# Optimization experiments

Hardware: AMD Instinct MI355X
Metric: run time of the kernel (lower is better)

## Reference

```python
import jax, jax.numpy as jnp
import numpy as np

X_DIM = 1024
HEADS = 16
EPS = 1e-5  # torch LayerNorm default


def setup_inputs() -> dict:
    key = jax.random.key(0)
    ks = jax.random.split(key, 4)
    B, N = 4, 1024
    x = jax.random.normal(ks[0], (B, N, X_DIM), jnp.float32)
    # torch nn.Linear weights are [out_features, in_features]; y = x @ W.T
    Wq = jax.random.normal(ks[1], (X_DIM, X_DIM), jnp.float32) * 0.02
    Wkv = jax.random.normal(ks[2], (2 * X_DIM, X_DIM), jnp.float32) * 0.02  # k_dim = x_dim + v_dim
    Wt = jax.random.normal(ks[3], (HEADS, HEADS), jnp.float32) * 0.25  # talk_h head-mixing
    ln_g = jnp.ones((HEADS,), jnp.float32)
    ln_b = jnp.zeros((HEADS,), jnp.float32)
    return {"x": x, "Wq": Wq, "Wkv": Wkv, "Wt": Wt, "ln_g": ln_g, "ln_b": ln_b}


def reference(x, Wq, Wkv, Wt, ln_g, ln_b):
    B, N, D = x.shape
    H = HEADS
    dh = D // H  # v head dim (= x head dim here since v_dim == x_dim)
    # projections
    q = (x @ Wq.T).reshape(B, N, H, dh).transpose(0, 2, 1, 3)  # b h i d
    kv = x @ Wkv.T  # [B, N, 2D]
    k = kv[..., :D].reshape(B, N, H, dh).transpose(0, 2, 1, 3)  # b h j d
    v = kv[..., D:].reshape(B, N, H, dh).transpose(0, 2, 1, 3)  # b h j d
    # scaled dot-product scores (scale uses x_dim, not head dim — faithful to source)
    dots = jnp.einsum('bhid,bhjd->bhij', q, k) * (D ** -0.5)
    w = jax.nn.softmax(dots, axis=-1)  # [B, H, N, N]
    # talk_h: ChSwap (transpose dims 1 and -1) -> Linear(heads) -> LayerNorm(heads) -> ChSwap
    wt = w.transpose(0, 3, 2, 1)  # b j i h
    wt = wt @ Wt.T
    mu = wt.mean(-1, keepdims=True)
    var = wt.var(-1, keepdims=True)
    wt = (wt - mu) / jnp.sqrt(var + EPS) * ln_g + ln_b
    w = wt.transpose(0, 3, 2, 1)  # back to b h i j
    # soft attention output
    attn = jnp.einsum('bhij,bhjd->bhid', w, v)
    # hard selection: argmax over keys, gather value rows
    idx = jnp.argmax(w, axis=-1)  # [B, H, N]
    hard = jnp.take_along_axis(v, jnp.broadcast_to(idx[..., None], idx.shape + (dh,)), axis=2)
    # straight-through: forward = hard, gradient flows through attn
    rtn = attn - jax.lax.stop_gradient(attn - hard)
    return rtn.transpose(0, 2, 1, 3).reshape(B, N, H * dh)
```

## Files before the change

kernel.cpp:

```cpp
#include <hip/hip_runtime.h>


#define FMA4(cc, av, bv) \
  cc.x = fmaf(av, bv.x, cc.x); cc.y = fmaf(av, bv.y, cc.y); \
  cc.z = fmaf(av, bv.z, cc.z); cc.w = fmaf(av, bv.w, cc.w);

__global__ __launch_bounds__(256) void qkv_gemm(
    const float* __restrict__ X, const float* __restrict__ Wq,
    const float* __restrict__ Wkv, float* __restrict__ qT,
    float* __restrict__ kT, float* __restrict__ V)
{
  __shared__ __align__(16) float As[16 * 132];
  __shared__ __align__(16) float Bs[16 * 132];
  __shared__ __align__(16) float tb[128 * 32];

  const int t  = threadIdx.x;
  const int bn = blockIdx.x;
  const int bm = blockIdx.y;
  const int m0 = bm * 128, n0 = bn * 128;
  const int ty = t >> 4, tx = t & 15;

  const float* Wbase = (n0 < 1024) ? Wq : Wkv;
  const int nw0 = (n0 < 1024) ? n0 : (n0 - 1024);

  float4 c2[8][2];
#pragma unroll
  for (int a = 0; a < 8; a++) {
    c2[a][0] = make_float4(0.f, 0.f, 0.f, 0.f);
    c2[a][1] = make_float4(0.f, 0.f, 0.f, 0.f);
  }

  const int lr = t >> 1;
  const int lh = t & 1;

  const float4* As4 = (const float4*)As;
  const float4* Bs4 = (const float4*)Bs;

  for (int kb = 0; kb < 64; kb++) {
    const int k0 = kb * 16;
    __syncthreads();
#pragma unroll
    for (int s = 0; s < 2; s++) {
      const int kk = lh * 8 + s * 4;
      float4 av = *(const float4*)&X[(size_t)(m0 + lr) * 1024 + k0 + kk];
      float4 bv = *(const float4*)&Wbase[(size_t)(nw0 + lr) * 1024 + k0 + kk];
      As[(kk + 0) * 132 + lr] = av.x;
      As[(kk + 1) * 132 + lr] = av.y;
      As[(kk + 2) * 132 + lr] = av.z;
      As[(kk + 3) * 132 + lr] = av.w;
      Bs[(kk + 0) * 132 + lr] = bv.x;
      Bs[(kk + 1) * 132 + lr] = bv.y;
      Bs[(kk + 2) * 132 + lr] = bv.z;
      Bs[(kk + 3) * 132 + lr] = bv.w;
    }
    __syncthreads();
#pragma unroll
    for (int kk = 0; kk < 16; kk++) {
      float4 a0 = As4[kk * 33 + ty * 2];
      float4 a1 = As4[kk * 33 + ty * 2 + 1];
      float4 b0 = Bs4[kk * 33 + tx];
      float4 b1 = Bs4[kk * 33 + 16 + tx];
      FMA4(c2[0][0], a0.x, b0); FMA4(c2[0][1], a0.x, b1);
      FMA4(c2[1][0], a0.y, b0); FMA4(c2[1][1], a0.y, b1);
      FMA4(c2[2][0], a0.z, b0); FMA4(c2[2][1], a0.z, b1);
      FMA4(c2[3][0], a0.w, b0); FMA4(c2[3][1], a0.w, b1);
      FMA4(c2[4][0], a1.x, b0); FMA4(c2[4][1], a1.x, b1);
      FMA4(c2[5][0], a1.y, b0); FMA4(c2[5][1], a1.y, b1);
      FMA4(c2[6][0], a1.z, b0); FMA4(c2[6][1], a1.z, b1);
      FMA4(c2[7][0], a1.w, b0); FMA4(c2[7][1], a1.w, b1);
    }
  }

  if (n0 >= 2048) {
    const int nv0 = n0 - 2048;
#pragma unroll
    for (int a = 0; a < 8; a++) {
      *(float4*)&V[(size_t)(m0 + ty * 8 + a) * 1024 + nv0 + tx * 4]      = c2[a][0];
      *(float4*)&V[(size_t)(m0 + ty * 8 + a) * 1024 + nv0 + 64 + tx * 4] = c2[a][1];
    }
    return;
  }

  float* T = (n0 < 1024) ? qT : kT;
  const int nt0 = (n0 < 1024) ? n0 : (n0 - 1024);
  const int bB = m0 >> 10;
  const int i0 = m0 & 1023;
#pragma unroll
  for (int r = 0; r < 4; r++) {
    __syncthreads();
    if ((tx >> 3) == (r & 1)) {
      const int c0 = (tx & 7) * 4;
#pragma unroll
      for (int a = 0; a < 8; a++) {
        const int m = ty * 8 + a;
        float4 val = c2[a][r >> 1];
        tb[m * 32 + ((c0 + 0 + m) & 31)] = val.x;
        tb[m * 32 + ((c0 + 1 + m) & 31)] = val.y;
        tb[m * 32 + ((c0 + 2 + m) & 31)] = val.z;
        tb[m * 32 + ((c0 + 3 + m) & 31)] = val.w;
      }
    }
    __syncthreads();
    const int nl = t >> 3, mq = t & 7;
    float* Trow = T + (size_t)(bB * 1024 + nt0 + (r >> 1) * 64 + (r & 1) * 32 + nl) * 1024 + i0;
#pragma unroll
    for (int l = 0; l < 4; l++) {
      const int mb = (l * 8 + mq) * 4;
      float4 o;
      o.x = tb[(mb + 0) * 32 + ((nl + mb + 0) & 31)];
      o.y = tb[(mb + 1) * 32 + ((nl + mb + 1) & 31)];
      o.z = tb[(mb + 2) * 32 + ((nl + mb + 2) & 31)];
      o.w = tb[(mb + 3) * 32 + ((nl + mb + 3) & 31)];
      *(float4*)(Trow + mb) = o;
    }
  }
}

__global__ __launch_bounds__(256) void attn_stats_v5(
    const float* __restrict__ qT, const float* __restrict__ kT,
    float* __restrict__ Mm, float* __restrict__ Ml)
{
  const int t  = threadIdx.x;
  const int bx = blockIdx.x;
  const int b  = bx >> 8;
  const int it = (bx >> 3) & 31;
  const int js = bx & 7;
  const int wv = t >> 6;
  const int l  = t & 63;
  const int ih = l >> 5;
  const int jg = l & 31;
  const int i0w = __builtin_amdgcn_readfirstlane(it * 32 + wv * 8);
  const int iq = i0w + ih * 4;
  const int jq = js * 128 + jg * 4;

  const float scale = 0.03125f;

  for (int h = 0; h < 16; h++) {
    const size_t base = (size_t)(b * 1024 + h * 64) * 1024;
    float4 acc[4];
#pragma unroll
    for (int ii = 0; ii < 4; ii++) acc[ii] = make_float4(0.f, 0.f, 0.f, 0.f);

#pragma unroll 4
    for (int d = 0; d < 64; d++) {
      const float4 qv = *(const float4*)(qT + base + (size_t)d * 1024 + iq);
      const float4 kv = *(const float4*)(kT + base + (size_t)d * 1024 + jq);
      FMA4(acc[0], qv.x, kv);
      FMA4(acc[1], qv.y, kv);
      FMA4(acc[2], qv.z, kv);
      FMA4(acc[3], qv.w, kv);
    }

#pragma unroll
    for (int ii = 0; ii < 4; ii++) {
      const float s0 = acc[ii].x * scale;
      const float s1 = acc[ii].y * scale;
      const float s2 = acc[ii].z * scale;
      const float s3 = acc[ii].w * scale;
      float mx = fmaxf(fmaxf(s0, s1), fmaxf(s2, s3));
      mx = fmaxf(mx, __shfl_xor(mx, 1));
      mx = fmaxf(mx, __shfl_xor(mx, 2));
      mx = fmaxf(mx, __shfl_xor(mx, 4));
      mx = fmaxf(mx, __shfl_xor(mx, 8));
      mx = fmaxf(mx, __shfl_xor(mx, 16));
      float ss = __expf(s0 - mx) + __expf(s1 - mx) +
                 __expf(s2 - mx) + __expf(s3 - mx);
      ss += __shfl_xor(ss, 1);
      ss += __shfl_xor(ss, 2);
      ss += __shfl_xor(ss, 4);
      ss += __shfl_xor(ss, 8);
      ss += __shfl_xor(ss, 16);
      if (jg == ii) {
        const int idx = (((b * 16 + h) * 1024 + iq + ii) << 3) + js;
        Mm[idx] = mx;
        Ml[idx] = ss;
      }
    }
  }
}

__device__ inline unsigned long long mkkey(float v, int j) {
  unsigned u = __float_as_uint(v);
  u = (u & 0x80000000u) ? ~u : (u | 0x80000000u);
  return ((unsigned long long)u << 32) | (unsigned)(1023 - j);
}

__global__ __launch_bounds__(256) void attn_select_v5(
    const float* __restrict__ qT, const float* __restrict__ kT,
    const float* __restrict__ Mm, const float* __restrict__ Ml,
    const float* __restrict__ Wt, const float* __restrict__ ln_g,
    const float* __restrict__ ln_b, unsigned long long* __restrict__ HiKey)
{
  __shared__ __align__(16) float smem[64 * 271 + 512];
  float* ptile = smem;
  float* mred  = smem + 64 * 271;
  float* rred  = mred + 256;

  const int t  = threadIdx.x;
  const int bx = blockIdx.x;
  const int b  = bx >> 10;
  const int it = (bx >> 4) & 63;
  const int js = bx & 15;
  const int i0 = it << 4;
  const int j0 = js << 6;

  const float scale = 0.03125f;

  {
    const int base = (((b * 16 + (t >> 4)) * 1024 + i0 + (t & 15)) << 3);
    const float4 ma = *(const float4*)&Mm[base];
    const float4 mb = *(const float4*)&Mm[base + 4];
    const float4 la = *(const float4*)&Ml[base];
    const float4 lb = *(const float4*)&Ml[base + 4];
    float M = fmaxf(fmaxf(fmaxf(ma.x, ma.y), fmaxf(ma.z, ma.w)),
                    fmaxf(fmaxf(mb.x, mb.y), fmaxf(mb.z, mb.w)));
    float L = la.x * __expf(ma.x - M) + la.y * __expf(ma.y - M) +
              la.z * __expf(ma.z - M) + la.w * __expf(ma.w - M) +
              lb.x * __expf(mb.x - M) + lb.y * __expf(mb.y - M) +
              lb.z * __expf(mb.z - M) + lb.w * __expf(mb.w - M);
    mred[t] = M;
    rred[t] = 1.0f / L;
  }
  __syncthreads();

  const int wv = t >> 6;
  const int l  = t & 63;
  const int jq = l & 15;
  const int ig = l >> 4;
  const int iq = i0 + ig * 4;
  const int jcol = j0 + jq * 4;

#pragma unroll
  for (int hl = 0; hl < 4; hl++) {
    const int h = wv * 4 + hl;
    const size_t base = (size_t)(b * 1024 + h * 64) * 1024;
    float4 acc[4];
#pragma unroll
    for (int ii = 0; ii < 4; ii++) acc[ii] = make_float4(0.f, 0.f, 0.f, 0.f);

#pragma unroll 4
    for (int d = 0; d < 64; d++) {
      const float4 qv = *(const float4*)(qT + base + (size_t)d * 1024 + iq);
      const float4 kv = *(const float4*)(kT + base + (size_t)d * 1024 + jcol);
      FMA4(acc[0], qv.x, kv);
      FMA4(acc[1], qv.y, kv);
      FMA4(acc[2], qv.z, kv);
      FMA4(acc[3], qv.w, kv);
    }

    const int hrot = (h + jq) & 15;
#pragma unroll
    for (int ii = 0; ii < 4; ii++) {
      const int iL = ig * 4 + ii;
      const float m = mred[h * 16 + iL];
      const float r = rred[h * 16 + iL];
      const float a4[4] = {acc[ii].x, acc[ii].y, acc[ii].z, acc[ii].w};
#pragma unroll
      for (int jj = 0; jj < 4; jj++) {
        const int j = jq * 4 + jj;
        const float p = __expf(a4[jj] * scale - m) * r;
        ptile[j * 271 + iL * 17 + hrot] = p;
      }
    }
  }
  __syncthreads();

  const int i2 = t >> 4;
  const int g  = (t >> 2) & 3;
  const int hq = t & 3;

  float wtr[4][16], gr[4], br[4];
#pragma unroll
  for (int a = 0; a < 4; a++) {
#pragma unroll
    for (int h2 = 0; h2 < 16; h2++) wtr[a][h2] = Wt[(hq * 4 + a) * 16 + h2];
    gr[a] = ln_g[hq * 4 + a];
    br[a] = ln_b[hq * 4 + a];
  }
  float bv[4]; int bix[4];
#pragma unroll
  for (int a = 0; a < 4; a++) { bv[a] = -1e30f; bix[a] = 0; }

#pragma unroll
  for (int jj = 0; jj < 16; jj++) {
    const int j = g * 16 + jj;
    const int jr = j >> 2;
    float pv[16];
#pragma unroll
    for (int h2 = 0; h2 < 16; h2++)
      pv[h2] = ptile[j * 271 + i2 * 17 + ((h2 + jr) & 15)];
    float mix[4];
#pragma unroll
    for (int a = 0; a < 4; a++) {
      float s0 = 0.f;
#pragma unroll
      for (int h2 = 0; h2 < 16; h2++) s0 = fmaf(pv[h2], wtr[a][h2], s0);
      mix[a] = s0;
    }
    float s1 = mix[0] + mix[1] + mix[2] + mix[3];
    s1 += __shfl_xor(s1, 1);
    s1 += __shfl_xor(s1, 2);
    const float mu = s1 * 0.0625f;
    float s2 = 0.f;
#pragma unroll
    for (int a = 0; a < 4; a++) { const float dd = mix[a] - mu; s2 = fmaf(dd, dd, s2); }
    s2 += __shfl_xor(s2, 1);
    s2 += __shfl_xor(s2, 2);
    const float rstd = rsqrtf(s2 * 0.0625f + 1e-5f);
    const int jg2 = j0 + j;
#pragma unroll
    for (int a = 0; a < 4; a++) {
      const float nv = (mix[a] - mu) * rstd * gr[a] + br[a];
      if (nv > bv[a]) { bv[a] = nv; bix[a] = jg2; }
    }
  }

#pragma unroll
  for (int a = 0; a < 4; a++) {
    float v = bv[a]; int ix = bix[a];
    {
      const float ov = __shfl_xor(v, 4);
      const int oi = __shfl_xor(ix, 4);
      if (ov > v || (ov == v && oi < ix)) { v = ov; ix = oi; }
    }
    {
      const float ov = __shfl_xor(v, 8);
      const int oi = __shfl_xor(ix, 8);
      if (ov > v || (ov == v && oi < ix)) { v = ov; ix = oi; }
    }
    bv[a] = v; bix[a] = ix;
  }

  if (g == 0) {
#pragma unroll
    for (int a = 0; a < 4; a++) {
      const int cell = (b * 16 + hq * 4 + a) * 1024 + i0 + i2;
      atomicMax(&HiKey[cell], mkkey(bv[a], bix[a]));
    }
  }
}

__global__ __launch_bounds__(256) void gather_v4(
    const unsigned long long* __restrict__ HiKey, const float* __restrict__ V,
    float* __restrict__ out)
{
  const int t  = threadIdx.x;
  const int bx = blockIdx.x;
  const int b  = bx >> 6;
  const int it = bx & 63;
  const int i2 = t >> 4;
  const int h  = t & 15;

  const unsigned long long key = HiKey[(b * 16 + h) * 1024 + it * 16 + i2];
  const int j = 1023 - (int)(unsigned)(key & 0xFFFFFFFFull);

  const float* vs = V + (size_t)(b * 1024 + j) * 1024 + h * 64;
  float* dst = out + (size_t)(b * 1024 + it * 16 + i2) * 1024 + h * 64;
#pragma unroll
  for (int w = 0; w < 16; w++)
    *(float4*)(dst + w * 4) = *(const float4*)(vs + w * 4);
}

extern "C" void kernel_launch(void* const* d_in, const int* in_sizes, int n_in,
                              void* d_out, int out_size, void* d_ws, size_t ws_size,
                              hipStream_t stream) {
  const float* x   = (const float*)d_in[0];
  const float* Wq  = (const float*)d_in[1];
  const float* Wkv = (const float*)d_in[2];
  const float* Wt  = (const float*)d_in[3];
  const float* lng = (const float*)d_in[4];
  const float* lnb = (const float*)d_in[5];
  float* out = (float*)d_out;
  float* ws  = (float*)d_ws;
  float* qT = ws;
  float* kT = ws + (size_t)4 * 1024 * 1024;
  float* V  = ws + (size_t)8 * 1024 * 1024;
  float* Mm = ws + (size_t)12 * 1024 * 1024;
  float* Ml = Mm + 524288;
  unsigned long long* HiKey =
      (unsigned long long*)(ws + (size_t)13 * 1024 * 1024);

  hipLaunchKernelGGL(qkv_gemm, dim3(24, 32), dim3(256), 0, stream,
                     x, Wq, Wkv, qT, kT, V);
  hipMemsetAsync(HiKey, 0, (size_t)65536 * 8, stream);
  hipLaunchKernelGGL(attn_stats_v5, dim3(1024), dim3(256), 0, stream,
                     qT, kT, Mm, Ml);
  hipLaunchKernelGGL(attn_select_v5, dim3(4096), dim3(256), 0, stream,
                     qT, kT, Mm, Ml, Wt, lng, lnb, HiKey);
  hipLaunchKernelGGL(gather_v4, dim3(256), dim3(256), 0, stream,
                     HiKey, V, out);
}
```

Measured before the change: 963.5 us.

## Hold K column in registers, read Q row-major, drop softmax max tracking

```diff
diff --git a/kernel.cpp b/kernel.cpp
--- a/kernel.cpp
+++ b/kernel.cpp
@@ -7,7 +7,7 @@
 
 __global__ __launch_bounds__(256) void qkv_gemm(
     const float* __restrict__ X, const float* __restrict__ Wq,
-    const float* __restrict__ Wkv, float* __restrict__ qT,
+    const float* __restrict__ Wkv, float* __restrict__ Q,
     float* __restrict__ kT, float* __restrict__ V)
 {
   __shared__ __align__(16) float As[16 * 132];
@@ -71,6 +71,14 @@
     }
   }
 
+  if (n0 < 1024) {
+#pragma unroll
+    for (int a = 0; a < 8; a++) {
+      *(float4*)&Q[(size_t)(m0 + ty * 8 + a) * 1024 + n0 + tx * 4]      = c2[a][0];
+      *(float4*)&Q[(size_t)(m0 + ty * 8 + a) * 1024 + n0 + 64 + tx * 4] = c2[a][1];
+    }
+    return;
+  }
   if (n0 >= 2048) {
     const int nv0 = n0 - 2048;
 #pragma unroll
@@ -81,8 +89,7 @@
     return;
   }
 
-  float* T = (n0 < 1024) ? qT : kT;
-  const int nt0 = (n0 < 1024) ? n0 : (n0 - 1024);
+  const int nt0 = n0 - 1024;
   const int bB = m0 >> 10;
   const int i0 = m0 & 1023;
 #pragma unroll
@@ -102,7 +109,7 @@
     }
     __syncthreads();
     const int nl = t >> 3, mq = t & 7;
-    float* Trow = T + (size_t)(bB * 1024 + nt0 + (r >> 1) * 64 + (r & 1) * 32 + nl) * 1024 + i0;
+    float* Trow = kT + (size_t)(bB * 1024 + nt0 + (r >> 1) * 64 + (r & 1) * 32 + nl) * 1024 + i0;
 #pragma unroll
     for (int l = 0; l < 4; l++) {
       const int mb = (l * 8 + mq) * 4;
@@ -116,67 +123,81 @@
   }
 }
 
-__global__ __launch_bounds__(256) void attn_stats_v5(
-    const float* __restrict__ qT, const float* __restrict__ kT,
-    float* __restrict__ Mm, float* __restrict__ Ml)
+__global__ __launch_bounds__(256) void attn_stats_v6(
+    const float* __restrict__ Q, const float* __restrict__ kT,
+    float* __restrict__ Lp)
 {
   const int t  = threadIdx.x;
   const int bx = blockIdx.x;
-  const int b  = bx >> 8;
-  const int it = (bx >> 3) & 31;
-  const int js = bx & 7;
-  const int wv = t >> 6;
+  const int b  = bx >> 10;
+  const int it = (bx >> 4) & 63;
+  const int jw = bx & 15;
+  const int wv = __builtin_amdgcn_readfirstlane(t >> 6);
   const int l  = t & 63;
-  const int ih = l >> 5;
-  const int jg = l & 31;
-  const int i0w = __builtin_amdgcn_readfirstlane(it * 32 + wv * 8);
-  const int iq = i0w + ih * 4;
-  const int jq = js * 128 + jg * 4;
-
+  const int i0 = it << 4;
+  const int j  = (jw << 6) + l;
   const float scale = 0.03125f;
 
-  for (int h = 0; h < 16; h++) {
-    const size_t base = (size_t)(b * 1024 + h * 64) * 1024;
-    float4 acc[4];
-#pragma unroll
-    for (int ii = 0; ii < 4; ii++) acc[ii] = make_float4(0.f, 0.f, 0.f, 0.f);
-
-#pragma unroll 4
-    for (int d = 0; d < 64; d++) {
-      const float4 qv = *(const float4*)(qT + base + (size_t)d * 1024 + iq);
-      const float4 kv = *(const float4*)(kT + base + (size_t)d * 1024 + jq);
-      FMA4(acc[0], qv.x, kv);
-      FMA4(acc[1], qv.y, kv);
-      FMA4(acc[2], qv.z, kv);
-      FMA4(acc[3], qv.w, kv);
-    }
-
-#pragma unroll
-    for (int ii = 0; ii < 4; ii++) {
-      const float s0 = acc[ii].x * scale;
-      const float s1 = acc[ii].y * scale;
-      const float s2 = acc[ii].z * scale;
-      const float s3 = acc[ii].w * scale;
-      float mx = fmaxf(fmaxf(s0, s1), fmaxf(s2, s3));
-      mx = fmaxf(mx, __shfl_xor(mx, 1));
-      mx = fmaxf(mx, __shfl_xor(mx, 2));
-      mx = fmaxf(mx, __shfl_xor(mx, 4));
-      mx = fmaxf(mx, __shfl_xor(mx, 8));
-      mx = fmaxf(mx, __shfl_xor(mx, 16));
-      float ss = __expf(s0 - mx) + __expf(s1 - mx) +
-                 __expf(s2 - mx) + __expf(s3 - mx);
-      ss += __shfl_xor(ss, 1);
-      ss += __shfl_xor(ss, 2);
-      ss += __shfl_xor(ss, 4);
-      ss += __shfl_xor(ss, 8);
-      ss += __shfl_xor(ss, 16);
-      if (jg == ii) {
-        const int idx = (((b * 16 + h) * 1024 + iq + ii) << 3) + js;
-        Mm[idx] = mx;
-        Ml[idx] = ss;
-      }
-    }
-  }
+  float kreg[64];
+#pragma unroll 1
+  for (int hl = 0; hl < 4; hl++) {
+    const int h = wv * 4 + hl;
+    const float* kb = kT + (size_t)(b * 1024 + h * 64) * 1024 + j;
+#pragma unroll
+    for (int d = 0; d < 64; d++) kreg[d] = kb[(size_t)d << 10];
+
+#pragma unroll 1
+    for (int ic = 0; ic < 4; ic++) {
+      const float* q0 = Q + (size_t)(b * 1024 + i0 + ic * 4) * 1024 + h * 64;
+      float a0 = 0.f, a1 = 0.f, a2 = 0.f, a3 = 0.f;
+#pragma unroll
+      for (int d4 = 0; d4 < 16; d4++) {
+        const float4 qa = *(const float4*)(q0 + d4 * 4);
+        const float4 qb = *(const float4*)(q0 + 1024 + d4 * 4);
+        const float4 qc = *(const float4*)(q0 + 2048 + d4 * 4);
+        const float4 qd = *(const float4*)(q0 + 3072 + d4 * 4);
+        const float k0 = kreg[d4 * 4 + 0], k1 = kreg[d4 * 4 + 1];
+        const float k2 = kreg[d4 * 4 + 2], k3 = kreg[d4 * 4 + 3];
+        a0 = fmaf(qa.x, k0, a0); a1 = fmaf(qb.x, k0, a1);
+        a2 = fmaf(qc.x, k0, a2); a3 = fmaf(qd.x, k0, a3);
+        a0 = fmaf(qa.y, k1, a0); a1 = fmaf(qb.y, k1, a1);
+        a2 = fmaf(qc.y, k1, a2); a3 = fmaf(qd.y, k1, a3);
+        a0 = fmaf(qa.z, k2, a0); a1 = fmaf(qb.z, k2, a1);
+        a2 = fmaf(qc.z, k2, a2); a3 = fmaf(qd.z, k2, a3);
+        a0 = fmaf(qa.w, k3, a0); a1 = fmaf(qb.w, k3, a1);
+        a2 = fmaf(qc.w, k3, a2); a3 = fmaf(qd.w, k3, a3);
+      }
+      float e0 = __expf(a0 * scale);
+      float e1 = __expf(a1 * scale);
+      float e2 = __expf(a2 * scale);
+      float e3 = __expf(a3 * scale);
+#pragma unroll
+      for (int st = 1; st < 64; st <<= 1) {
+        e0 += __shfl_xor(e0, st);
+        e1 += __shfl_xor(e1, st);
+        e2 += __shfl_xor(e2, st);
+        e3 += __shfl_xor(e3, st);
+      }
+      if (l == 0) {
+        const int row = (b * 16 + h) * 1024 + i0 + ic * 4;
+        Lp[(size_t)(row + 0) * 16 + jw] = e0;
+        Lp[(size_t)(row + 1) * 16 + jw] = e1;
+        Lp[(size_t)(row + 2) * 16 + jw] = e2;
+        Lp[(size_t)(row + 3) * 16 + jw] = e3;
+      }
+    }
+  }
+}
+
+__global__ __launch_bounds__(256) void merge_l(
+    const float* __restrict__ Lp, float* __restrict__ Rl)
+{
+  const int idx = blockIdx.x * 256 + threadIdx.x;
+  const float4* p = (const float4*)(Lp + (size_t)idx * 16);
+  const float4 a = p[0], b4 = p[1], c = p[2], d = p[3];
+  const float s = ((((a.x + a.y) + (a.z + a.w)) + ((b4.x + b4.y) + (b4.z + b4.w)))
+                 + (((c.x + c.y) + (c.z + c.w)) + ((d.x + d.y) + (d.z + d.w))));
+  Rl[idx] = 1.0f / s;
 }
 
 __device__ inline unsigned long long mkkey(float v, int j) {
@@ -185,16 +206,13 @@
   return ((unsigned long long)u << 32) | (unsigned)(1023 - j);
 }
 
-__global__ __launch_bounds__(256) void attn_select_v5(
-    const float* __restrict__ qT, const float* __restrict__ kT,
-    const float* __restrict__ Mm, const float* __restrict__ Ml,
-    const float* __restrict__ Wt, const float* __restrict__ ln_g,
-    const float* __restrict__ ln_b, unsigned long long* __restrict__ HiKey)
-{
-  __shared__ __align__(16) float smem[64 * 271 + 512];
-  float* ptile = smem;
-  float* mred  = smem + 64 * 271;
-  float* rred  = mred + 256;
+__global__ __launch_bounds__(256) void attn_select_v6(
+    const float* __restrict__ Q, const float* __restrict__ kT,
+    const float* __restrict__ Rl, const float* __restrict__ Wt,
+    const float* __restrict__ ln_g, const float* __restrict__ ln_b,
+    unsigned long long* __restrict__ HiKey)
+{
+  __shared__ __align__(16) float ptile[64 * 271];
 
   const int t  = threadIdx.x;
   const int bx = blockIdx.x;
@@ -203,64 +221,45 @@
   const int js = bx & 15;
   const int i0 = it << 4;
   const int j0 = js << 6;
-
+  const int wv = __builtin_amdgcn_readfirstlane(t >> 6);
+  const int l  = t & 63;
   const float scale = 0.03125f;
 
-  {
-    const int base = (((b * 16 + (t >> 4)) * 1024 + i0 + (t & 15)) << 3);
-    const float4 ma = *(const float4*)&Mm[base];
-    const float4 mb = *(const float4*)&Mm[base + 4];
-    const float4 la = *(const float4*)&Ml[base];
-    const float4 lb = *(const float4*)&Ml[base + 4];
-    float M = fmaxf(fmaxf(fmaxf(ma.x, ma.y), fmaxf(ma.z, ma.w)),
-                    fmaxf(fmaxf(mb.x, mb.y), fmaxf(mb.z, mb.w)));
-    float L = la.x * __expf(ma.x - M) + la.y * __expf(ma.y - M) +
-              la.z * __expf(ma.z - M) + la.w * __expf(ma.w - M) +
-              lb.x * __expf(mb.x - M) + lb.y * __expf(mb.y - M) +
-              lb.z * __expf(mb.z - M) + lb.w * __expf(mb.w - M);
-    mred[t] = M;
-    rred[t] = 1.0f / L;
-  }
-  __syncthreads();
-
-  const int wv = t >> 6;
-  const int l  = t & 63;
-  const int jq = l & 15;
-  const int ig = l >> 4;
-  const int iq = i0 + ig * 4;
-  const int jcol = j0 + jq * 4;
-
-#pragma unroll
+  float kreg[64];
+#pragma unroll 1
   for (int hl = 0; hl < 4; hl++) {
     const int h = wv * 4 + hl;
-    const size_t base = (size_t)(b * 1024 + h * 64) * 1024;
-    float4 acc[4];
-#pragma unroll
-    for (int ii = 0; ii < 4; ii++) acc[ii] = make_float4(0.f, 0.f, 0.f, 0.f);
-
-#pragma unroll 4
-    for (int d = 0; d < 64; d++) {
-      const float4 qv = *(const float4*)(qT + base + (size_t)d * 1024 + iq);
-      const float4 kv = *(const float4*)(kT + base + (size_t)d * 1024 + jcol);
-      FMA4(acc[0], qv.x, kv);
-      FMA4(acc[1], qv.y, kv);
-      FMA4(acc[2], qv.z, kv);
-      FMA4(acc[3], qv.w, kv);
-    }
-
-    const int hrot = (h + jq) & 15;
-#pragma unroll
-    for (int ii = 0; ii < 4; ii++) {
-      const int iL = ig * 4 + ii;
-      const float m = mred[h * 16 + iL];
-      const float r = rred[h * 16 + iL];
-      const float a4[4] = {acc[ii].x, acc[ii].y, acc[ii].z, acc[ii].w};
-#pragma unroll
-      for (int jj = 0; jj < 4; jj++) {
-        const int j = jq * 4 + jj;
-        const float p = __expf(a4[jj] * scale - m) * r;
-        ptile[j * 271 + iL * 17 + hrot] = p;
-      }
+    const float* kb = kT + (size_t)(b * 1024 + h * 64) * 1024 + j0 + l;
+#pragma unroll
+    for (int d = 0; d < 64; d++) kreg[d] = kb[(size_t)d << 10];
+
+#pragma unroll 1
+    for (int ic = 0; ic < 4; ic++) {
+      const float* q0 = Q + (size_t)(b * 1024 + i0 + ic * 4) * 1024 + h * 64;
+      const float4 rlv = *(const float4*)(Rl + (b * 16 + h) * 1024 + i0 + ic * 4);
+      float a0 = 0.f, a1 = 0.f, a2 = 0.f, a3 = 0.f;
+#pragma unroll
+      for (int d4 = 0; d4 < 16; d4++) {
+        const float4 qa = *(const float4*)(q0 + d4 * 4);
+        const float4 qb = *(const float4*)(q0 + 1024 + d4 * 4);
+        const float4 qc = *(const float4*)(q0 + 2048 + d4 * 4);
+        const float4 qd = *(const float4*)(q0 + 3072 + d4 * 4);
+        const float k0 = kreg[d4 * 4 + 0], k1 = kreg[d4 * 4 + 1];
+        const float k2 = kreg[d4 * 4 + 2], k3 = kreg[d4 * 4 + 3];
+        a0 = fmaf(qa.x, k0, a0); a1 = fmaf(qb.x, k0, a1);
+        a2 = fmaf(qc.x, k0, a2); a3 = fmaf(qd.x, k0, a3);
+        a0 = fmaf(qa.y, k1, a0); a1 = fmaf(qb.y, k1, a1);
+        a2 = fmaf(qc.y, k1, a2); a3 = fmaf(qd.y, k1, a3);
+        a0 = fmaf(qa.z, k2, a0); a1 = fmaf(qb.z, k2, a1);
+        a2 = fmaf(qc.z, k2, a2); a3 = fmaf(qd.z, k2, a3);
+        a0 = fmaf(qa.w, k3, a0); a1 = fmaf(qb.w, k3, a1);
+        a2 = fmaf(qc.w, k3, a2); a3 = fmaf(qd.w, k3, a3);
+      }
+      const int iL = ic * 4;
+      ptile[l * 271 + (iL + 0) * 17 + h] = __expf(a0 * scale) * rlv.x;
+      ptile[l * 271 + (iL + 1) * 17 + h] = __expf(a1 * scale) * rlv.y;
+      ptile[l * 271 + (iL + 2) * 17 + h] = __expf(a2 * scale) * rlv.z;
+      ptile[l * 271 + (iL + 3) * 17 + h] = __expf(a3 * scale) * rlv.w;
     }
   }
   __syncthreads();
@@ -284,11 +283,9 @@
 #pragma unroll
   for (int jj = 0; jj < 16; jj++) {
     const int j = g * 16 + jj;
-    const int jr = j >> 2;
     float pv[16];
 #pragma unroll
-    for (int h2 = 0; h2 < 16; h2++)
-      pv[h2] = ptile[j * 271 + i2 * 17 + ((h2 + jr) & 15)];
+    for (int h2 = 0; h2 < 16; h2++) pv[h2] = ptile[j * 271 + i2 * 17 + h2];
     float mix[4];
 #pragma unroll
     for (int a = 0; a < 4; a++) {
@@ -372,21 +369,22 @@
   const float* lnb = (const float*)d_in[5];
   float* out = (float*)d_out;
   float* ws  = (float*)d_ws;
-  float* qT = ws;
+  float* Q  = ws;
   float* kT = ws + (size_t)4 * 1024 * 1024;
   float* V  = ws + (size_t)8 * 1024 * 1024;
-  float* Mm = ws + (size_t)12 * 1024 * 1024;
-  float* Ml = Mm + 524288;
+  float* Lp = ws + (size_t)12 * 1024 * 1024;
+  float* Rl = ws + (size_t)13 * 1024 * 1024;
   unsigned long long* HiKey =
-      (unsigned long long*)(ws + (size_t)13 * 1024 * 1024);
+      (unsigned long long*)(ws + (size_t)13 * 1024 * 1024 + 131072);
 
   hipLaunchKernelGGL(qkv_gemm, dim3(24, 32), dim3(256), 0, stream,
-                     x, Wq, Wkv, qT, kT, V);
+                     x, Wq, Wkv, Q, kT, V);
   hipMemsetAsync(HiKey, 0, (size_t)65536 * 8, stream);
-  hipLaunchKernelGGL(attn_stats_v5, dim3(1024), dim3(256), 0, stream,
-                     qT, kT, Mm, Ml);
-  hipLaunchKernelGGL(attn_select_v5, dim3(4096), dim3(256), 0, stream,
-                     qT, kT, Mm, Ml, Wt, lng, lnb, HiKey);
+  hipLaunchKernelGGL(attn_stats_v6, dim3(4096), dim3(256), 0, stream,
+                     Q, kT, Lp);
+  hipLaunchKernelGGL(merge_l, dim3(256), dim3(256), 0, stream, Lp, Rl);
+  hipLaunchKernelGGL(attn_select_v6, dim3(4096), dim3(256), 0, stream,
+                     Q, kT, Rl, Wt, lng, lnb, HiKey);
   hipLaunchKernelGGL(gather_v4, dim3(256), dim3(256), 0, stream,
                      HiKey, V, out);
 }
```

Measured after the change: 1.200 ms. 24.5% more time.

## Split stats kernel over head groups and halve select kernel's shared tile

Applied to the files above, without the earlier changes.

```diff
diff --git a/kernel.cpp b/kernel.cpp
--- a/kernel.cpp
+++ b/kernel.cpp
@@ -116,15 +116,16 @@
   }
 }
 
-__global__ __launch_bounds__(256) void attn_stats_v5(
+__global__ __launch_bounds__(256) void attn_stats_v7(
     const float* __restrict__ qT, const float* __restrict__ kT,
     float* __restrict__ Mm, float* __restrict__ Ml)
 {
   const int t  = threadIdx.x;
   const int bx = blockIdx.x;
-  const int b  = bx >> 8;
-  const int it = (bx >> 3) & 31;
-  const int js = bx & 7;
+  const int b  = bx >> 10;
+  const int it = (bx >> 5) & 31;
+  const int js = (bx >> 2) & 7;
+  const int hg = bx & 3;
   const int wv = t >> 6;
   const int l  = t & 63;
   const int ih = l >> 5;
@@ -135,7 +136,8 @@
 
   const float scale = 0.03125f;
 
-  for (int h = 0; h < 16; h++) {
+  for (int hl = 0; hl < 4; hl++) {
+    const int h = hg * 4 + hl;
     const size_t base = (size_t)(b * 1024 + h * 64) * 1024;
     float4 acc[4];
 #pragma unroll
@@ -185,15 +187,15 @@
   return ((unsigned long long)u << 32) | (unsigned)(1023 - j);
 }
 
-__global__ __launch_bounds__(256) void attn_select_v5(
+__global__ __launch_bounds__(256, 4) void attn_select_v7(
     const float* __restrict__ qT, const float* __restrict__ kT,
     const float* __restrict__ Mm, const float* __restrict__ Ml,
     const float* __restrict__ Wt, const float* __restrict__ ln_g,
     const float* __restrict__ ln_b, unsigned long long* __restrict__ HiKey)
 {
-  __shared__ __align__(16) float smem[64 * 271 + 512];
+  __shared__ __align__(16) float smem[32 * 271 + 512];
   float* ptile = smem;
-  float* mred  = smem + 64 * 271;
+  float* mred  = smem + 32 * 271;
   float* rred  = mred + 256;
 
   const int t  = threadIdx.x;
@@ -223,47 +225,12 @@
   }
   __syncthreads();
 
-  const int wv = t >> 6;
+  const int wv = __builtin_amdgcn_readfirstlane(t >> 6);
   const int l  = t & 63;
-  const int jq = l & 15;
-  const int ig = l >> 4;
+  const int hh = l >> 5;
+  const int ig = (l >> 3) & 3;
+  const int jq = l & 7;
   const int iq = i0 + ig * 4;
-  const int jcol = j0 + jq * 4;
-
-#pragma unroll
-  for (int hl = 0; hl < 4; hl++) {
-    const int h = wv * 4 + hl;
-    const size_t base = (size_t)(b * 1024 + h * 64) * 1024;
-    float4 acc[4];
-#pragma unroll
-    for (int ii = 0; ii < 4; ii++) acc[ii] = make_float4(0.f, 0.f, 0.f, 0.f);
-
-#pragma unroll 4
-    for (int d = 0; d < 64; d++) {
-      const float4 qv = *(const float4*)(qT + base + (size_t)d * 1024 + iq);
-      const float4 kv = *(const float4*)(kT + base + (size_t)d * 1024 + jcol);
-      FMA4(acc[0], qv.x, kv);
-      FMA4(acc[1], qv.y, kv);
-      FMA4(acc[2], qv.z, kv);
-      FMA4(acc[3], qv.w, kv);
-    }
-
-    const int hrot = (h + jq) & 15;
-#pragma unroll
-    for (int ii = 0; ii < 4; ii++) {
-      const int iL = ig * 4 + ii;
-      const float m = mred[h * 16 + iL];
-      const float r = rred[h * 16 + iL];
-      const float a4[4] = {acc[ii].x, acc[ii].y, acc[ii].z, acc[ii].w};
-#pragma unroll
-      for (int jj = 0; jj < 4; jj++) {
-        const int j = jq * 4 + jj;
-        const float p = __expf(a4[jj] * scale - m) * r;
-        ptile[j * 271 + iL * 17 + hrot] = p;
-      }
-    }
-  }
-  __syncthreads();
 
   const int i2 = t >> 4;
   const int g  = (t >> 2) & 3;
@@ -281,38 +248,74 @@
 #pragma unroll
   for (int a = 0; a < 4; a++) { bv[a] = -1e30f; bix[a] = 0; }
 
-#pragma unroll
-  for (int jj = 0; jj < 16; jj++) {
-    const int j = g * 16 + jj;
-    const int jr = j >> 2;
-    float pv[16];
-#pragma unroll
-    for (int h2 = 0; h2 < 16; h2++)
-      pv[h2] = ptile[j * 271 + i2 * 17 + ((h2 + jr) & 15)];
-    float mix[4];
-#pragma unroll
-    for (int a = 0; a < 4; a++) {
-      float s0 = 0.f;
-#pragma unroll
-      for (int h2 = 0; h2 < 16; h2++) s0 = fmaf(pv[h2], wtr[a][h2], s0);
-      mix[a] = s0;
-    }
-    float s1 = mix[0] + mix[1] + mix[2] + mix[3];
-    s1 += __shfl_xor(s1, 1);
-    s1 += __shfl_xor(s1, 2);
-    const float mu = s1 * 0.0625f;
-    float s2 = 0.f;
-#pragma unroll
-    for (int a = 0; a < 4; a++) { const float dd = mix[a] - mu; s2 = fmaf(dd, dd, s2); }
-    s2 += __shfl_xor(s2, 1);
-    s2 += __shfl_xor(s2, 2);
-    const float rstd = rsqrtf(s2 * 0.0625f + 1e-5f);
-    const int jg2 = j0 + j;
-#pragma unroll
-    for (int a = 0; a < 4; a++) {
-      const float nv = (mix[a] - mu) * rstd * gr[a] + br[a];
-      if (nv > bv[a]) { bv[a] = nv; bix[a] = jg2; }
-    }
+  for (int jh = 0; jh < 2; jh++) {
+    const int jcol = j0 + jh * 32 + jq * 4;
+
+#pragma unroll
+    for (int hl = 0; hl < 2; hl++) {
+      const int h = wv * 4 + hl * 2 + hh;
+      const size_t base = (size_t)(b * 1024 + h * 64) * 1024;
+      float4 acc[4];
+#pragma unroll
+      for (int ii = 0; ii < 4; ii++) acc[ii] = make_float4(0.f, 0.f, 0.f, 0.f);
+
+#pragma unroll 4
+      for (int d = 0; d < 64; d++) {
+        const float4 qv = *(const float4*)(qT + base + (size_t)d * 1024 + iq);
+        const float4 kv = *(const float4*)(kT + base + (size_t)d * 1024 + jcol);
+        FMA4(acc[0], qv.x, kv);
+        FMA4(acc[1], qv.y, kv);
+        FMA4(acc[2], qv.z, kv);
+        FMA4(acc[3], qv.w, kv);
+      }
+
+#pragma unroll
+      for (int ii = 0; ii < 4; ii++) {
+        const int iL = ig * 4 + ii;
+        const float m = mred[h * 16 + iL];
+        const float r = rred[h * 16 + iL];
+        const float a4[4] = {acc[ii].x, acc[ii].y, acc[ii].z, acc[ii].w};
+#pragma unroll
+        for (int jj = 0; jj < 4; jj++) {
+          const float p = __expf(a4[jj] * scale - m) * r;
+          ptile[(jq * 4 + jj) * 271 + iL * 17 + h] = p;
+        }
+      }
+    }
+    __syncthreads();
+
+#pragma unroll
+    for (int jj = 0; jj < 8; jj++) {
+      const int jloc = g * 8 + jj;
+      float pv[16];
+#pragma unroll
+      for (int h2 = 0; h2 < 16; h2++) pv[h2] = ptile[jloc * 271 + i2 * 17 + h2];
+      float mix[4];
+#pragma unroll
+      for (int a = 0; a < 4; a++) {
+        float s0 = 0.f;
+#pragma unroll
+        for (int h2 = 0; h2 < 16; h2++) s0 = fmaf(pv[h2], wtr[a][h2], s0);
+        mix[a] = s0;
+      }
+      float s1 = mix[0] + mix[1] + mix[2] + mix[3];
+      s1 += __shfl_xor(s1, 1);
+      s1 += __shfl_xor(s1, 2);
+      const float mu = s1 * 0.0625f;
+      float s2 = 0.f;
+#pragma unroll
+      for (int a = 0; a < 4; a++) { const float dd = mix[a] - mu; s2 = fmaf(dd, dd, s2); }
+      s2 += __shfl_xor(s2, 1);
+      s2 += __shfl_xor(s2, 2);
+      const float rstd = rsqrtf(s2 * 0.0625f + 1e-5f);
+      const int jg2 = j0 + jh * 32 + jloc;
+#pragma unroll
+      for (int a = 0; a < 4; a++) {
+        const float nv = (mix[a] - mu) * rstd * gr[a] + br[a];
+        if (nv > bv[a]) { bv[a] = nv; bix[a] = jg2; }
+      }
+    }
+    __syncthreads();
   }
 
 #pragma unroll
@@ -383,9 +386,9 @@
   hipLaunchKernelGGL(qkv_gemm, dim3(24, 32), dim3(256), 0, stream,
                      x, Wq, Wkv, qT, kT, V);
   hipMemsetAsync(HiKey, 0, (size_t)65536 * 8, stream);
-  hipLaunchKernelGGL(attn_stats_v5, dim3(1024), dim3(256), 0, stream,
+  hipLaunchKernelGGL(attn_stats_v7, dim3(4096), dim3(256), 0, stream,
                      qT, kT, Mm, Ml);
-  hipLaunchKernelGGL(attn_select_v5, dim3(4096), dim3(256), 0, stream,
+  hipLaunchKernelGGL(attn_select_v7, dim3(4096), dim3(256), 0, stream,
                      qT, kT, Mm, Ml, Wt, lng, lnb, HiKey);
   hipLaunchKernelGGL(gather_v4, dim3(256), dim3(256), 0, stream,
                      HiKey, V, out);
```

New measurement: 1.266 ms. 1.31x slower.
